# Kernel tuning notes

Hardware: AMD Instinct MI355X
Metric: run time of the kernel (lower is better)

## Reference

```python
import jax, jax.numpy as jnp
import numpy as np

CLAMP_MIN, CLAMP_MAX = -60.0, 30.0


def setup_inputs() -> dict:
    key = jax.random.key(0)
    k1, k2, k3, k4 = jax.random.split(key, 4)
    b, n, d = 8, 4096, 512
    x = jax.random.normal(k1, (b, n, d), dtype=jnp.float32)
    pos = jax.random.normal(k2, (n - 1,), dtype=jnp.float32)
    zero = jax.random.normal(k3, (1,), dtype=jnp.float32)
    neg = jax.random.normal(k4, (n - 1,), dtype=jnp.float32)
    return {"x": x, "pos": pos, "zero": zero, "neg": neg}


def reference(x, pos, zero, neg):
    # ToepliztV2.forward with dim=1, normalize=False, use_exp=True,
    # type_num=-1, causal=False, and seq_len n == self.n (so l1=n-1, l2=0
    # and the -inf padding of pos/neg is empty).
    n = x.shape[1]
    # kernel of length 2n: [zero, pos, zero, neg], exp(clamp(.))
    a = jnp.exp(jnp.clip(jnp.concatenate([zero, pos, zero, neg]), CLAMP_MIN, CLAMP_MAX))
    # compute(): zero-padded FFT conv. x fft/ifft use ortho norm, kernel fft
    # uses default (backward) norm, matching the torch code exactly.
    y = jnp.fft.fft(x, 2 * n, axis=1, norm="ortho")          # [b, 2n, d] complex
    v = jnp.fft.fft(a)[None, :, None]                          # [1, 2n, 1] complex
    out = jnp.fft.ifft(v * y, 2 * n, axis=1, norm="ortho")[:, :n, :].real
    return out
```

## Files before the change

### kernel.cpp

```cpp
#include <hip/hip_runtime.h>
#include <hip/hip_bf16.h>
#include <stdint.h>

#define NSEQ 4096
#define DDIM 512
#define NB   8
#define FN   8192

#define PADI(i) ((i) + ((i) >> 4))

struct __align__(8) cf { float x, y; };

__device__ __forceinline__ cf cadd(cf a, cf b) { return {a.x + b.x, a.y + b.y}; }
__device__ __forceinline__ cf csub(cf a, cf b) { return {a.x - b.x, a.y - b.y}; }
__device__ __forceinline__ cf cmul(cf a, cf b) {
    return {a.x * b.x - a.y * b.y, a.x * b.y + a.y * b.x};
}
__device__ __forceinline__ cf cmulc(cf a, cf b) {
    return {a.x * b.x + a.y * b.y, a.y * b.x - a.x * b.y};
}
template<int DIR> __device__ __forceinline__ cf crot(cf z) {
    return DIR < 0 ? cf{z.y, -z.x} : cf{-z.y, z.x};
}

__device__ __forceinline__ unsigned short f2bf(float f) {
    union { float f; unsigned int u; } v;
    v.f = f;
    unsigned int u = v.u;
    u += 0x7FFFu + ((u >> 16) & 1u);
    return (unsigned short)(u >> 16);
}
__device__ __forceinline__ float bf2f(unsigned short u) {
    union { unsigned int i; float f; } v;
    v.i = (unsigned int)u << 16;
    return v.f;
}

template<int DIR>
__device__ __forceinline__ void fft4(cf& b0, cf& b1, cf& b2, cf& b3) {
    cf s0 = cadd(b0, b2), s1 = csub(b0, b2);
    cf s2 = cadd(b1, b3), s3 = crot<DIR>(csub(b1, b3));
    b0 = cadd(s0, s2); b1 = cadd(s1, s3);
    b2 = csub(s0, s2); b3 = csub(s1, s3);
}

template<int DIR>
__device__ __forceinline__ void dft8(cf a[8]) {
    cf e0 = a[0], e1 = a[2], e2 = a[4], e3 = a[6];
    cf o0 = a[1], o1 = a[3], o2 = a[5], o3 = a[7];
    fft4<DIR>(e0, e1, e2, e3);
    fft4<DIR>(o0, o1, o2, o3);
    const float c = 0.70710678118654752f;
    cf w1 = (DIR < 0) ? cf{c, -c} : cf{c, c};
    cf w3 = (DIR < 0) ? cf{-c, -c} : cf{-c, c};
    o1 = cmul(o1, w1);
    o2 = crot<DIR>(o2);
    o3 = cmul(o3, w3);
    a[0] = cadd(e0, o0); a[1] = cadd(e1, o1); a[2] = cadd(e2, o2); a[3] = cadd(e3, o3);
    a[4] = csub(e0, o0); a[5] = csub(e1, o1); a[6] = csub(e2, o2); a[7] = csub(e3, o3);
}

template<int DIR>
__device__ __forceinline__ void dft8_half(cf a0, cf a1, cf a2, cf a3, cf a[8]) {
    cf r2 = crot<DIR>(a2), r3 = crot<DIR>(a3);
    cf e0 = cadd(a0, a2), e1 = cadd(a0, r2), e2 = csub(a0, a2), e3 = csub(a0, r2);
    cf o0 = cadd(a1, a3), o1 = cadd(a1, r3), o2 = csub(a1, a3), o3 = csub(a1, r3);
    const float c = 0.70710678118654752f;
    cf w1 = (DIR < 0) ? cf{c, -c} : cf{c, c};
    cf w3 = (DIR < 0) ? cf{-c, -c} : cf{-c, c};
    o1 = cmul(o1, w1);
    o2 = crot<DIR>(o2);
    o3 = cmul(o3, w3);
    a[0] = cadd(e0, o0); a[1] = cadd(e1, o1); a[2] = cadd(e2, o2); a[3] = cadd(e3, o3);
    a[4] = csub(e0, o0); a[5] = csub(e1, o1); a[6] = csub(e2, o2); a[7] = csub(e3, o3);
}

__device__ __forceinline__ void twpow(cf w1, cf w[8]) {
    w[1] = w1;
    w[2] = cmul(w1, w1);
    w[3] = cmul(w[2], w1);
    w[4] = cmul(w[2], w[2]);
    w[5] = cmul(w[4], w1);
    w[6] = cmul(w[4], w[2]);
    w[7] = cmul(w[4], w[3]);
}

template<int DIR, int LM, int TMUL>
__device__ __forceinline__ void r8_stage_tab(cf* Z, const cf* W7, int tid) {
    const int m = 1 << LM;
#pragma unroll
    for (int q = 0; q < 2; ++q) {
        int beta = q * 512 + tid;
        int j = beta & (m - 1);
        int g = beta >> LM;
        int base = (g << (LM + 3)) + j;
        cf a[8];
#pragma unroll
        for (int r = 0; r < 8; ++r) a[r] = Z[PADI(base + (r << LM))];
        cf w[8];
#pragma unroll
        for (int k = 1; k < 8; ++k) w[k] = W7[j * TMUL + k - 1];
        if (DIR > 0) {
#pragma unroll
            for (int k = 1; k < 8; ++k) a[k] = cmulc(a[k], w[k]);
        }
        dft8<DIR>(a);
        if (DIR < 0) {
#pragma unroll
            for (int k = 1; k < 8; ++k) a[k] = cmul(a[k], w[k]);
        }
#pragma unroll
        for (int r = 0; r < 8; ++r) Z[PADI(base + (r << LM))] = a[r];
    }
}

template<int NTHR>
__device__ __forceinline__ void r2_stage(cf* Z, int tid) {
#pragma unroll
    for (int q = 0; q < 4096 / NTHR; ++q) {
        int beta = q * NTHR + tid;
        int i0 = PADI(2 * beta), i1 = i0 + 1;
        cf a = Z[i0], b = Z[i1];
        Z[i0] = cadd(a, b);
        Z[i1] = csub(a, b);
    }
}

template<int DIR, int NTHR>
__device__ __forceinline__ void r8_stage(cf* Z, int lm, int tid) {
    const int m = 1 << lm;
    const float ang0 = ((DIR < 0) ? -6.2831853071795865f : 6.2831853071795865f)
                       / (float)(m * 8);
#pragma unroll
    for (int q = 0; q < 1024 / NTHR; ++q) {
        int beta = q * NTHR + tid;
        int j = beta & (m - 1);
        int g = beta >> lm;
        int base = (g << (lm + 3)) + j;
        cf a[8];
#pragma unroll
        for (int r = 0; r < 8; ++r) a[r] = Z[PADI(base + (r << lm))];
        float sn, cs;
        __sincosf(ang0 * (float)j, &sn, &cs);
        cf w[8];
        twpow({cs, sn}, w);
        if (DIR > 0) {
#pragma unroll
            for (int k = 1; k < 8; ++k) a[k] = cmul(a[k], w[k]);
        }
        dft8<DIR>(a);
        if (DIR < 0) {
#pragma unroll
            for (int k = 1; k < 8; ++k) a[k] = cmul(a[k], w[k]);
        }
#pragma unroll
        for (int r = 0; r < 8; ++r) Z[PADI(base + (r << lm))] = a[r];
    }
}

__global__ __launch_bounds__(512) void prep(const float* __restrict__ x,
                                            const float* __restrict__ pos,
                                            const float* __restrict__ zero,
                                            const float* __restrict__ neg,
                                            unsigned short* __restrict__ xT,
                                            float4* __restrict__ Vt4) {
    __shared__ cf Z[PADI(FN)];
    int tid = threadIdx.x;
    if (blockIdx.x == 0) {
        float zv = zero[0];
#pragma unroll
        for (int q = 0; q < 16; ++q) {
            int t = q * 512 + tid;
            float v;
            if (t == 0 || t == NSEQ) v = zv;
            else if (t < NSEQ)       v = pos[t - 1];
            else                     v = neg[t - NSEQ - 1];
            v = fminf(fmaxf(v, -60.0f), 30.0f);
            Z[PADI(t)] = {__expf(v), 0.0f};
        }
        __syncthreads();
        r8_stage<-1, 512>(Z, 10, tid); __syncthreads();
        r8_stage<-1, 512>(Z, 7,  tid); __syncthreads();
        r8_stage<-1, 512>(Z, 4,  tid); __syncthreads();
        r8_stage<-1, 512>(Z, 1,  tid); __syncthreads();
        r2_stage<512>(Z, tid);         __syncthreads();
        const float sc = 1.0f / (float)FN;
#pragma unroll
        for (int q = 0; q < 16; ++q) {
            int i = q * 512 + tid;
            int p = i >> 1, r = p & 7;
            cf V0 = Z[PADI(2 * p)], V1 = Z[PADI(2 * p + 1)];
            cf Vp = {(V0.x + V1.x) * sc, (V0.y + V1.y) * sc};
            cf Vm = {(V0.x - V1.x) * sc, (V0.y - V1.y) * sc};
            float sn, cs;
            __sincosf(-0.39269908169872415f * (float)r, &sn, &cs);
            cf wf = {cs, sn};
            cf B = (i & 1) ? cmulc(Vm, wf) : cmul(Vm, wf);
            Vt4[i] = {Vp.x, Vp.y, B.x, B.y};
        }
    } else {
        unsigned short (*tl)[72] = (unsigned short (*)[72])Z;
        int t   = blockIdx.x - 1;
        int b   = t >> 9;
        int rem = t & 511;
        int j0  = (rem >> 3) << 6;
        int d0  = (rem & 7) << 6;
        const float* xb = x + (size_t)b * NSEQ * DDIM;
#pragma unroll
        for (int e = 0; e < 2; ++e) {
            int idx = e * 512 + tid;
            int r   = idx >> 4;
            int c4  = (idx & 15) << 2;
            float4 v = *(const float4*)&xb[(size_t)(j0 + r) * DDIM + d0 + c4];
            ushort4 o;
            o.x = f2bf(v.x); o.y = f2bf(v.y); o.z = f2bf(v.z); o.w = f2bf(v.w);
            *(ushort4*)&tl[r][c4] = o;
        }
        __syncthreads();
        unsigned short* xtb = xT + (size_t)b * DDIM * NSEQ;
#pragma unroll
        for (int e = 0; e < 2; ++e) {
            int idx = e * 512 + tid;
            int d   = idx >> 4;
            int jq  = (idx & 15) << 2;
            ushort4 o;
            o.x = tl[jq + 0][d]; o.y = tl[jq + 1][d];
            o.z = tl[jq + 2][d]; o.w = tl[jq + 3][d];
            *(ushort4*)&xtb[(size_t)(d0 + d) * NSEQ + j0 + jq] = o;
        }
    }
}

__global__ __launch_bounds__(512, 4) void fft_conv(unsigned short* __restrict__ xT,
                                                   const float4* __restrict__ Vt4) {
    __shared__ cf Z[PADI(FN)];
    __shared__ cf Wt[512];
    __shared__ cf W7[896];
    int tid = threadIdx.x;
    int blk = blockIdx.x;
    int b   = blk >> 8;
    int dp  = blk & 255;
    unsigned short* col0 = xT + ((size_t)(b * DDIM + 2 * dp)) * NSEQ;
    unsigned short* col1 = col0 + NSEQ;

    {
        float sn, cs;
        __sincosf(-7.66990393942820625e-04f * (float)tid, &sn, &cs);
        Wt[tid] = {cs, sn};
        int e = tid;
        int t8 = e / 7, k = e - t8 * 7 + 1;
        __sincosf(-6.13592315154256492e-03f * (float)(t8 * k), &sn, &cs);
        W7[e] = {cs, sn};
        if (tid < 384) {
            e = tid + 512;
            t8 = e / 7; k = e - t8 * 7 + 1;
            __sincosf(-6.13592315154256492e-03f * (float)(t8 * k), &sn, &cs);
            W7[e] = {cs, sn};
        }
    }
    __syncthreads();

    const cf KF = {0.92387953251128674f, -0.38268343236508977f};

#pragma unroll
    for (int q = 0; q < 2; ++q) {
        int j = q * 512 + tid;
        cf a0 = {bf2f(col0[j]),        bf2f(col1[j])};
        cf a1 = {bf2f(col0[j + 1024]), bf2f(col1[j + 1024])};
        cf a2 = {bf2f(col0[j + 2048]), bf2f(col1[j + 2048])};
        cf a3 = {bf2f(col0[j + 3072]), bf2f(col1[j + 3072])};
        cf a[8];
        dft8_half<-1>(a0, a1, a2, a3, a);
        cf w1 = Wt[tid];
        if (q == 1) w1 = cmul(w1, KF);
        cf w[8];
        twpow(w1, w);
#pragma unroll
        for (int k = 1; k < 8; ++k) a[k] = cmul(a[k], w[k]);
#pragma unroll
        for (int r = 0; r < 8; ++r) Z[PADI(j + (r << 10))] = a[r];
    }
    __syncthreads();

    r8_stage_tab<-1, 7, 7>(Z, W7, tid);   __syncthreads();
    r8_stage_tab<-1, 4, 56>(Z, W7, tid);  __syncthreads();

#pragma unroll
    for (int q = 0; q < 2; ++q) {
        const int idx = q * 512 + tid;
        const int g  = idx >> 1;
        const int jj = idx & 1;
        const int base = g * 16 + jj;
        cf a[8];
#pragma unroll
        for (int r = 0; r < 8; ++r) a[r] = Z[PADI(base + 2 * r)];
        dft8<-1>(a);
#pragma unroll
        for (int r = 0; r < 8; ++r) {
            cf own = a[r];
            cf oth;
            oth.x = __shfl_xor(own.x, 1);
            oth.y = __shfl_xor(own.y, 1);
            float4 v = Vt4[base + 2 * r];
            a[r] = cadd(cmul({v.x, v.y}, own), cmul({v.z, v.w}, oth));
        }
        dft8<1>(a);
#pragma unroll
        for (int r = 0; r < 8; ++r) Z[PADI(base + 2 * r)] = a[r];
    }
    __syncthreads();

    r8_stage_tab<1, 4, 56>(Z, W7, tid);   __syncthreads();
    r8_stage_tab<1, 7, 7>(Z, W7, tid);    __syncthreads();

#pragma unroll
    for (int q = 0; q < 2; ++q) {
        int j = q * 512 + tid;
        cf a[8];
#pragma unroll
        for (int r = 0; r < 8; ++r) a[r] = Z[PADI(j + (r << 10))];
        cf w1 = Wt[tid];
        if (q == 1) w1 = cmul(w1, KF);
        w1.y = -w1.y;
        cf w[8];
        twpow(w1, w);
#pragma unroll
        for (int k = 1; k < 8; ++k) a[k] = cmul(a[k], w[k]);
        dft8<1>(a);
#pragma unroll
        for (int r = 0; r < 4; ++r) {
            col0[j + (r << 10)] = f2bf(a[r].x);
            col1[j + (r << 10)] = f2bf(a[r].y);
        }
    }
}

__global__ void untranspose(const unsigned short* __restrict__ oT,
                            float* __restrict__ out) {
    __shared__ unsigned short tl[64][65];
    int j0 = blockIdx.x * 64, d0 = blockIdx.y * 64, b = blockIdx.z;
    const unsigned short* src = oT + (size_t)b * DDIM * NSEQ;
#pragma unroll
    for (int e = 0; e < 16; ++e) {
        int idx = e * 256 + threadIdx.x;
        int r = idx >> 6, c = idx & 63;
        tl[r][c] = src[(size_t)(d0 + r) * NSEQ + j0 + c];
    }
    __syncthreads();
    float* dst = out + ((size_t)b * NSEQ + j0) * DDIM + d0;
#pragma unroll
    for (int e = 0; e < 16; ++e) {
        int idx = e * 256 + threadIdx.x;
        int r = idx >> 6, c = idx & 63;
        dst[(size_t)r * DDIM + c] = bf2f(tl[c][r]);
    }
}

extern "C" void kernel_launch(void* const* d_in, const int* in_sizes, int n_in,
                              void* d_out, int out_size, void* d_ws, size_t ws_size,
                              hipStream_t stream) {
    const float* x    = (const float*)d_in[0];
    const float* pos  = (const float*)d_in[1];
    const float* zero = (const float*)d_in[2];
    const float* neg  = (const float*)d_in[3];
    float* out = (float*)d_out;

    unsigned short* xT = (unsigned short*)d_ws;
    float4* Vt = (float4*)((char*)d_ws + (size_t)32 * 1024 * 1024);

    prep<<<dim3(4097), 512, 0, stream>>>(x, pos, zero, neg, xT, Vt);
    fft_conv<<<dim3(NB * 256), 512, 0, stream>>>(xT, Vt);
    untranspose<<<dim3(64, 8, 8), 256, 0, stream>>>(xT, out);
}
```

Measured before the change: 97.48 us.

## Switch FFT decomposition from radix-8 to radix-16 stages

Replaces the radix-8 FFT stages (4 radix-8 plus a radix-2 pass) with three radix-16 stages built from two radix-8 butterflies. This applies to both the kernel-spectrum prep and the per-column convolution FFT. Each thread now processes one 16-point butterfly instead of two 8-point ones, so there are fewer shared-memory passes and barriers, and the twiddle table shrinks. The cost is higher register pressure from 16-element arrays under launch_bounds(512,4), which may cause spills or lower occupancy.

```diff
diff --git a/kernel.cpp b/kernel.cpp
--- a/kernel.cpp
+++ b/kernel.cpp
@@ -75,7 +75,48 @@
     a[4] = csub(e0, o0); a[5] = csub(e1, o1); a[6] = csub(e2, o2); a[7] = csub(e3, o3);
 }
 
-__device__ __forceinline__ void twpow(cf w1, cf w[8]) {
+template<int DIR>
+__device__ __forceinline__ void comb16(cf e[8], cf o[8], cf a[16]) {
+    const float C8 = 0.92387953251128674f, S8 = 0.38268343236508977f;
+    const float c  = 0.70710678118654752f;
+    cf u1 = (DIR < 0) ? cf{C8, -S8} : cf{C8, S8};
+    cf u2 = (DIR < 0) ? cf{c, -c}   : cf{c, c};
+    cf u3 = (DIR < 0) ? cf{S8, -C8} : cf{S8, C8};
+    cf u5 = (DIR < 0) ? cf{-S8, -C8} : cf{-S8, C8};
+    cf u6 = (DIR < 0) ? cf{-c, -c}  : cf{-c, c};
+    cf u7 = (DIR < 0) ? cf{-C8, -S8} : cf{-C8, S8};
+    o[1] = cmul(o[1], u1);
+    o[2] = cmul(o[2], u2);
+    o[3] = cmul(o[3], u3);
+    o[4] = crot<DIR>(o[4]);
+    o[5] = cmul(o[5], u5);
+    o[6] = cmul(o[6], u6);
+    o[7] = cmul(o[7], u7);
+#pragma unroll
+    for (int t = 0; t < 8; ++t) {
+        a[t]     = cadd(e[t], o[t]);
+        a[t + 8] = csub(e[t], o[t]);
+    }
+}
+
+template<int DIR>
+__device__ __forceinline__ void dft16(cf a[16]) {
+    cf e[8] = {a[0], a[2], a[4], a[6], a[8], a[10], a[12], a[14]};
+    cf o[8] = {a[1], a[3], a[5], a[7], a[9], a[11], a[13], a[15]};
+    dft8<DIR>(e);
+    dft8<DIR>(o);
+    comb16<DIR>(e, o, a);
+}
+
+template<int DIR>
+__device__ __forceinline__ void dft16_half(cf b[8], cf a[16]) {
+    cf e[8], o[8];
+    dft8_half<DIR>(b[0], b[2], b[4], b[6], e);
+    dft8_half<DIR>(b[1], b[3], b[5], b[7], o);
+    comb16<DIR>(e, o, a);
+}
+
+__device__ __forceinline__ void twpow15(cf w1, cf w[16]) {
     w[1] = w1;
     w[2] = cmul(w1, w1);
     w[3] = cmul(w[2], w1);
@@ -83,35 +124,9 @@
     w[5] = cmul(w[4], w1);
     w[6] = cmul(w[4], w[2]);
     w[7] = cmul(w[4], w[3]);
-}
-
-template<int DIR, int LM, int TMUL>
-__device__ __forceinline__ void r8_stage_tab(cf* Z, const cf* W7, int tid) {
-    const int m = 1 << LM;
-#pragma unroll
-    for (int q = 0; q < 2; ++q) {
-        int beta = q * 512 + tid;
-        int j = beta & (m - 1);
-        int g = beta >> LM;
-        int base = (g << (LM + 3)) + j;
-        cf a[8];
-#pragma unroll
-        for (int r = 0; r < 8; ++r) a[r] = Z[PADI(base + (r << LM))];
-        cf w[8];
-#pragma unroll
-        for (int k = 1; k < 8; ++k) w[k] = W7[j * TMUL + k - 1];
-        if (DIR > 0) {
-#pragma unroll
-            for (int k = 1; k < 8; ++k) a[k] = cmulc(a[k], w[k]);
-        }
-        dft8<DIR>(a);
-        if (DIR < 0) {
-#pragma unroll
-            for (int k = 1; k < 8; ++k) a[k] = cmul(a[k], w[k]);
-        }
-#pragma unroll
-        for (int r = 0; r < 8; ++r) Z[PADI(base + (r << LM))] = a[r];
-    }
+    w[8] = cmul(w[4], w[4]);
+#pragma unroll
+    for (int k = 9; k < 16; ++k) w[k] = cmul(w[8], w[k - 8]);
 }
 
 template<int NTHR>
@@ -123,38 +138,6 @@
         cf a = Z[i0], b = Z[i1];
         Z[i0] = cadd(a, b);
         Z[i1] = csub(a, b);
-    }
-}
-
-template<int DIR, int NTHR>
-__device__ __forceinline__ void r8_stage(cf* Z, int lm, int tid) {
-    const int m = 1 << lm;
-    const float ang0 = ((DIR < 0) ? -6.2831853071795865f : 6.2831853071795865f)
-                       / (float)(m * 8);
-#pragma unroll
-    for (int q = 0; q < 1024 / NTHR; ++q) {
-        int beta = q * NTHR + tid;
-        int j = beta & (m - 1);
-        int g = beta >> lm;
-        int base = (g << (lm + 3)) + j;
-        cf a[8];
-#pragma unroll
-        for (int r = 0; r < 8; ++r) a[r] = Z[PADI(base + (r << lm))];
-        float sn, cs;
-        __sincosf(ang0 * (float)j, &sn, &cs);
-        cf w[8];
-        twpow({cs, sn}, w);
-        if (DIR > 0) {
-#pragma unroll
-            for (int k = 1; k < 8; ++k) a[k] = cmul(a[k], w[k]);
-        }
-        dft8<DIR>(a);
-        if (DIR < 0) {
-#pragma unroll
-            for (int k = 1; k < 8; ++k) a[k] = cmul(a[k], w[k]);
-        }
-#pragma unroll
-        for (int r = 0; r < 8; ++r) Z[PADI(base + (r << lm))] = a[r];
     }
 }
 
@@ -179,21 +162,68 @@
             Z[PADI(t)] = {__expf(v), 0.0f};
         }
         __syncthreads();
-        r8_stage<-1, 512>(Z, 10, tid); __syncthreads();
-        r8_stage<-1, 512>(Z, 7,  tid); __syncthreads();
-        r8_stage<-1, 512>(Z, 4,  tid); __syncthreads();
-        r8_stage<-1, 512>(Z, 1,  tid); __syncthreads();
-        r2_stage<512>(Z, tid);         __syncthreads();
+        {
+            int j = tid;
+            cf a[16];
+#pragma unroll
+            for (int r = 0; r < 16; ++r) a[r] = Z[PADI(j + (r << 9))];
+            dft16<-1>(a);
+            float sn, cs;
+            __sincosf(-7.66990393942820625e-04f * (float)j, &sn, &cs);
+            cf w[16];
+            twpow15({cs, sn}, w);
+#pragma unroll
+            for (int t = 1; t < 16; ++t) a[t] = cmul(a[t], w[t]);
+#pragma unroll
+            for (int t = 0; t < 16; ++t) Z[PADI(j + (t << 9))] = a[t];
+        }
+        __syncthreads();
+        {
+            int j = tid & 31, g = tid >> 5;
+            int base = (g << 9) + j;
+            cf a[16];
+#pragma unroll
+            for (int r = 0; r < 16; ++r) a[r] = Z[PADI(base + (r << 5))];
+            dft16<-1>(a);
+            float sn, cs;
+            __sincosf(-1.22718463030851298e-02f * (float)j, &sn, &cs);
+            cf w[16];
+            twpow15({cs, sn}, w);
+#pragma unroll
+            for (int t = 1; t < 16; ++t) a[t] = cmul(a[t], w[t]);
+#pragma unroll
+            for (int t = 0; t < 16; ++t) Z[PADI(base + (t << 5))] = a[t];
+        }
+        __syncthreads();
+        {
+            int jj = tid & 1, g = tid >> 1;
+            int base = g * 32 + jj;
+            cf a[16];
+#pragma unroll
+            for (int r = 0; r < 16; ++r) a[r] = Z[PADI(base + 2 * r)];
+            dft16<-1>(a);
+            if (jj) {
+                cf w[16];
+                twpow15({0.98078528040323044f, -0.19509032201612827f}, w);
+#pragma unroll
+                for (int t = 1; t < 16; ++t) a[t] = cmul(a[t], w[t]);
+            }
+#pragma unroll
+            for (int t = 0; t < 16; ++t) Z[PADI(base + 2 * t)] = a[t];
+        }
+        __syncthreads();
+        r2_stage<512>(Z, tid);
+        __syncthreads();
         const float sc = 1.0f / (float)FN;
 #pragma unroll
         for (int q = 0; q < 16; ++q) {
             int i = q * 512 + tid;
-            int p = i >> 1, r = p & 7;
+            int p = i >> 1, t = p & 15;
             cf V0 = Z[PADI(2 * p)], V1 = Z[PADI(2 * p + 1)];
             cf Vp = {(V0.x + V1.x) * sc, (V0.y + V1.y) * sc};
             cf Vm = {(V0.x - V1.x) * sc, (V0.y - V1.y) * sc};
             float sn, cs;
-            __sincosf(-0.39269908169872415f * (float)r, &sn, &cs);
+            __sincosf(-0.19634954084936207f * (float)t, &sn, &cs);
             cf wf = {cs, sn};
             cf B = (i & 1) ? cmulc(Vm, wf) : cmul(Vm, wf);
             Vt4[i] = {Vp.x, Vp.y, B.x, B.y};
@@ -235,7 +265,7 @@
                                                    const float4* __restrict__ Vt4) {
     __shared__ cf Z[PADI(FN)];
     __shared__ cf Wt[512];
-    __shared__ cf W7[896];
+    __shared__ cf W15[480];
     int tid = threadIdx.x;
     int blk = blockIdx.x;
     int b   = blk >> 8;
@@ -247,90 +277,97 @@
         float sn, cs;
         __sincosf(-7.66990393942820625e-04f * (float)tid, &sn, &cs);
         Wt[tid] = {cs, sn};
-        int e = tid;
-        int t8 = e / 7, k = e - t8 * 7 + 1;
-        __sincosf(-6.13592315154256492e-03f * (float)(t8 * k), &sn, &cs);
-        W7[e] = {cs, sn};
-        if (tid < 384) {
-            e = tid + 512;
-            t8 = e / 7; k = e - t8 * 7 + 1;
-            __sincosf(-6.13592315154256492e-03f * (float)(t8 * k), &sn, &cs);
-            W7[e] = {cs, sn};
-        }
-    }
-    __syncthreads();
-
-    const cf KF = {0.92387953251128674f, -0.38268343236508977f};
-
-#pragma unroll
-    for (int q = 0; q < 2; ++q) {
-        int j = q * 512 + tid;
-        cf a0 = {bf2f(col0[j]),        bf2f(col1[j])};
-        cf a1 = {bf2f(col0[j + 1024]), bf2f(col1[j + 1024])};
-        cf a2 = {bf2f(col0[j + 2048]), bf2f(col1[j + 2048])};
-        cf a3 = {bf2f(col0[j + 3072]), bf2f(col1[j + 3072])};
-        cf a[8];
-        dft8_half<-1>(a0, a1, a2, a3, a);
-        cf w1 = Wt[tid];
-        if (q == 1) w1 = cmul(w1, KF);
-        cf w[8];
-        twpow(w1, w);
-#pragma unroll
-        for (int k = 1; k < 8; ++k) a[k] = cmul(a[k], w[k]);
-#pragma unroll
-        for (int r = 0; r < 8; ++r) Z[PADI(j + (r << 10))] = a[r];
-    }
-    __syncthreads();
-
-    r8_stage_tab<-1, 7, 7>(Z, W7, tid);   __syncthreads();
-    r8_stage_tab<-1, 4, 56>(Z, W7, tid);  __syncthreads();
-
-#pragma unroll
-    for (int q = 0; q < 2; ++q) {
-        const int idx = q * 512 + tid;
-        const int g  = idx >> 1;
-        const int jj = idx & 1;
-        const int base = g * 16 + jj;
-        cf a[8];
-#pragma unroll
-        for (int r = 0; r < 8; ++r) a[r] = Z[PADI(base + 2 * r)];
-        dft8<-1>(a);
-#pragma unroll
-        for (int r = 0; r < 8; ++r) {
-            cf own = a[r];
+        if (tid < 480) {
+            int j = tid / 15, t = tid - j * 15 + 1;
+            __sincosf(-1.22718463030851298e-02f * (float)(j * t), &sn, &cs);
+            W15[tid] = {cs, sn};
+        }
+    }
+    __syncthreads();
+
+    {
+        int j = tid;
+        cf bb[8];
+#pragma unroll
+        for (int r = 0; r < 8; ++r)
+            bb[r] = {bf2f(col0[j + (r << 9)]), bf2f(col1[j + (r << 9)])};
+        cf a[16];
+        dft16_half<-1>(bb, a);
+        cf w[16];
+        twpow15(Wt[j], w);
+#pragma unroll
+        for (int t = 1; t < 16; ++t) a[t] = cmul(a[t], w[t]);
+#pragma unroll
+        for (int t = 0; t < 16; ++t) Z[PADI(j + (t << 9))] = a[t];
+    }
+    __syncthreads();
+
+    {
+        int j = tid & 31, g = tid >> 5;
+        int base = (g << 9) + j;
+        cf a[16];
+#pragma unroll
+        for (int r = 0; r < 16; ++r) a[r] = Z[PADI(base + (r << 5))];
+        dft16<-1>(a);
+#pragma unroll
+        for (int t = 1; t < 16; ++t) a[t] = cmul(a[t], W15[j * 15 + t - 1]);
+#pragma unroll
+        for (int t = 0; t < 16; ++t) Z[PADI(base + (t << 5))] = a[t];
+    }
+    __syncthreads();
+
+    {
+        int jj = tid & 1, g = tid >> 1;
+        int base = g * 32 + jj;
+        cf a[16];
+#pragma unroll
+        for (int r = 0; r < 16; ++r) a[r] = Z[PADI(base + 2 * r)];
+        dft16<-1>(a);
+#pragma unroll
+        for (int t = 0; t < 16; ++t) {
+            cf own = a[t];
             cf oth;
             oth.x = __shfl_xor(own.x, 1);
             oth.y = __shfl_xor(own.y, 1);
-            float4 v = Vt4[base + 2 * r];
-            a[r] = cadd(cmul({v.x, v.y}, own), cmul({v.z, v.w}, oth));
-        }
-        dft8<1>(a);
-#pragma unroll
-        for (int r = 0; r < 8; ++r) Z[PADI(base + 2 * r)] = a[r];
-    }
-    __syncthreads();
-
-    r8_stage_tab<1, 4, 56>(Z, W7, tid);   __syncthreads();
-    r8_stage_tab<1, 7, 7>(Z, W7, tid);    __syncthreads();
-
-#pragma unroll
-    for (int q = 0; q < 2; ++q) {
-        int j = q * 512 + tid;
-        cf a[8];
-#pragma unroll
-        for (int r = 0; r < 8; ++r) a[r] = Z[PADI(j + (r << 10))];
-        cf w1 = Wt[tid];
-        if (q == 1) w1 = cmul(w1, KF);
+            float4 v = Vt4[base + 2 * t];
+            a[t] = cadd(cmul({v.x, v.y}, own), cmul({v.z, v.w}, oth));
+        }
+        dft16<1>(a);
+#pragma unroll
+        for (int t = 0; t < 16; ++t) Z[PADI(base + 2 * t)] = a[t];
+    }
+    __syncthreads();
+
+    {
+        int j = tid & 31, g = tid >> 5;
+        int base = (g << 9) + j;
+        cf a[16];
+#pragma unroll
+        for (int r = 0; r < 16; ++r) a[r] = Z[PADI(base + (r << 5))];
+#pragma unroll
+        for (int t = 1; t < 16; ++t) a[t] = cmulc(a[t], W15[j * 15 + t - 1]);
+        dft16<1>(a);
+#pragma unroll
+        for (int t = 0; t < 16; ++t) Z[PADI(base + (t << 5))] = a[t];
+    }
+    __syncthreads();
+
+    {
+        int j = tid;
+        cf a[16];
+#pragma unroll
+        for (int t = 0; t < 16; ++t) a[t] = Z[PADI(j + (t << 9))];
+        cf w1 = Wt[j];
         w1.y = -w1.y;
-        cf w[8];
-        twpow(w1, w);
-#pragma unroll
-        for (int k = 1; k < 8; ++k) a[k] = cmul(a[k], w[k]);
-        dft8<1>(a);
-#pragma unroll
-        for (int r = 0; r < 4; ++r) {
-            col0[j + (r << 10)] = f2bf(a[r].x);
-            col1[j + (r << 10)] = f2bf(a[r].y);
+        cf w[16];
+        twpow15(w1, w);
+#pragma unroll
+        for (int t = 1; t < 16; ++t) a[t] = cmul(a[t], w[t]);
+        dft16<1>(a);
+#pragma unroll
+        for (int r = 0; r < 8; ++r) {
+            col0[j + (r << 9)] = f2bf(a[r].x);
+            col1[j + (r << 9)] = f2bf(a[r].y);
         }
     }
 }
```

Result: slower. 131.3 us (+34.7%).
